# Kernel tuning notes

Hardware: AMD Instinct MI355X
Metric: run time of the kernel (lower is better)

The kernel has to match this reference:

```python
import jax, jax.numpy as jnp
import numpy as np

N = 50000      # nodes
E = 1600000    # edges (avg degree 32)
C_IN = 128
C_H = 128
C_OUT = 10
G = 512        # number of graphs in the batch


def setup_inputs() -> dict:
    key = jax.random.key(0)
    ks = jax.random.split(key, 16)
    x = jax.random.normal(ks[0], (N, C_IN), dtype=jnp.float32)
    edge_index = jax.random.randint(ks[1], (2, E), 0, N, dtype=jnp.int64)
    batch = jnp.sort(jax.random.randint(ks[2], (N,), 0, G, dtype=jnp.int64))

    def lin(k, fan_in, fan_out):
        lim = 1.0 / np.sqrt(fan_in)
        return jax.random.uniform(k, (fan_in, fan_out), jnp.float32, -lim, lim)

    return {
        "x": x, "edge_index": edge_index, "batch": batch,
        # conv1: c_in -> c_hidden
        "Wr1": lin(ks[3], C_IN, C_H), "br1": jnp.zeros((C_H,), jnp.float32),
        "Wo1": lin(ks[4], C_IN, C_H),
        # conv2: c_hidden -> 2*c_hidden
        "Wr2": lin(ks[5], C_H, 2 * C_H), "br2": jnp.zeros((2 * C_H,), jnp.float32),
        "Wo2": lin(ks[6], C_H, 2 * C_H),
        # conv3: 2*c_hidden -> c_hidden
        "Wr3": lin(ks[7], 2 * C_H, C_H), "br3": jnp.zeros((C_H,), jnp.float32),
        "Wo3": lin(ks[8], 2 * C_H, C_H),
        # head
        "W1": lin(ks[9], C_H, 4 * C_OUT), "b1": jnp.zeros((4 * C_OUT,), jnp.float32),
        "W2": lin(ks[10], 4 * C_OUT, C_OUT), "b2": jnp.zeros((C_OUT,), jnp.float32),
    }


def _graph_conv(x, src, dst, Wr, br, Wo):
    # PyG GraphConv: lin_rel(sum_{j in N(i)} x_j) + lin_root(x_i)
    agg = jax.ops.segment_sum(x[src], dst, num_segments=N)  # [N, F_in]
    return agg @ Wr + br + x @ Wo


def reference(x, edge_index, batch, Wr1, br1, Wo1, Wr2, br2, Wo2,
              Wr3, br3, Wo3, W1, b1, W2, b2):
    src, dst = edge_index[0], edge_index[1]
    h = jax.nn.relu(_graph_conv(x, src, dst, Wr1, br1, Wo1))
    h = jax.nn.relu(_graph_conv(h, src, dst, Wr2, br2, Wo2))
    h = _graph_conv(h, src, dst, Wr3, br3, Wo3)
    # global mean pool over graphs
    sums = jax.ops.segment_sum(h, batch, num_segments=G)            # [G, C_H]
    cnts = jax.ops.segment_sum(jnp.ones((N,), h.dtype), batch, num_segments=G)
    pooled = sums / jnp.maximum(cnts, 1.0)[:, None]
    # dropout is identity in eval mode
    out = pooled @ W1 + b1
    out = out @ W2 + b2
    return out
```

## Files before the change

kernel.cpp:

```cpp
#include <hip/hip_runtime.h>
#include <hip/hip_bf16.h>
#include <cstddef>

#define NN 50000
#define EE 1600000
#define GG 512
#define NB 196
#define BSTRIDE 16384
#define BCAP 10240
#define XBLKS 6250
#define SCBLKS 782

typedef unsigned int u32;
typedef unsigned short u16;
typedef __attribute__((ext_vector_type(8))) short frag_ab;
typedef __attribute__((ext_vector_type(4))) float frag_cd;

__device__ __forceinline__ void gl_lds16(const void* g, void* l) {
    __builtin_amdgcn_global_load_lds(
        (const __attribute__((address_space(1))) u32*)g,
        (__attribute__((address_space(3))) u32*)l, 16, 0, 0);
}
__device__ __forceinline__ float b2f_lo(u32 v) { return __uint_as_float(v << 16); }
__device__ __forceinline__ float b2f_hi(u32 v) { return __uint_as_float(v & 0xffff0000u); }
__device__ __forceinline__ float b2f(u32 v, int odd) { return odd ? b2f_hi(v) : b2f_lo(v); }
__device__ __forceinline__ u16 f2b(float x) {
    __hip_bfloat16 h = __float2bfloat16(x);
    return *(u16*)&h;
}
__device__ __forceinline__ u32 pack2(float lo, float hi) {
    return ((u32)f2b(hi) << 16) | f2b(lo);
}
__device__ __forceinline__ void acc2(float2& a, u32 v) {
    a.x += b2f_lo(v);
    a.y += b2f_hi(v);
}


__global__ __launch_bounds__(256) void bscatter_prep_kernel(
    const int* __restrict__ ei, int* __restrict__ bcnt, u32* __restrict__ pairs,
    const float* __restrict__ x, u16* __restrict__ ax,
    const float* __restrict__ Wr1, const float* __restrict__ Wo1,
    const float* __restrict__ Wr2, const float* __restrict__ Wo2,
    const float* __restrict__ Wr3, const float* __restrict__ Wo3,
    const float* __restrict__ br3,
    u16* __restrict__ BT1, u16* __restrict__ BT2, u16* __restrict__ BT3,
    float* __restrict__ bias3) {
    __shared__ int lcnt[NB];
    __shared__ int lbase[NB];
    __shared__ unsigned short lpos[2048];
    int bid = blockIdx.x, t = threadIdx.x;
    if (bid < SCBLKS) {
        int e0 = bid * 2048;
        u32 pk[8];
        int bk[8];
        for (int i = t; i < NB; i += 256) lcnt[i] = 0;
        __syncthreads();
#pragma unroll
        for (int i = 0; i < 8; ++i) {
            int e = e0 + i * 256 + t;
            if (e < EE) {
                int dst = ei[EE + e], src = ei[e];
                int b = dst >> 8;
                bk[i] = b;
                pk[i] = ((u32)src << 8) | (u32)(dst & 255);
                lpos[i * 256 + t] = (unsigned short)atomicAdd(&lcnt[b], 1);
            } else bk[i] = -1;
        }
        __syncthreads();
        for (int i = t; i < NB; i += 256) lbase[i] = atomicAdd(&bcnt[i], lcnt[i]);
        __syncthreads();
#pragma unroll
        for (int i = 0; i < 8; ++i) {
            if (bk[i] >= 0) {
                int pos = lbase[bk[i]] + (int)lpos[i * 256 + t];
                pairs[(size_t)bk[i] * BSTRIDE + pos] = pk[i];
            }
        }
    } else if (bid < SCBLKS + XBLKS) {
        int idx = (bid - SCBLKS) * 256 + t;
        int row = idx >> 5, q = idx & 31;
        float4 v = *(const float4*)(x + (size_t)row * 128 + q * 4);
        *(u32*)(ax + (size_t)row * 256 + 128 + q * 4) = pack2(v.x, v.y);
        *(u32*)(ax + (size_t)row * 256 + 128 + q * 4 + 2) = pack2(v.z, v.w);
    } else {
        int m = bid - SCBLKS - XBLKS;
        int k = t;
        BT2[m * 256 + k] = f2b(k < 128 ? Wr2[k * 256 + m] : Wo2[(k - 128) * 256 + m]);
        BT3[m * 256 + k] = f2b(m < 128 ? Wr3[k * 128 + m] : Wo3[k * 128 + (m - 128)]);
        if (m < 128)
            BT1[m * 256 + k] = f2b(k < 128 ? Wr1[k * 128 + m] : Wo1[(k - 128) * 128 + m]);
        if (k == 0) bias3[m] = (m < 128) ? 0.f : br3[m - 128];
    }
}


__global__ __launch_bounds__(512) void bfill_kernel(const u32* __restrict__ pairs,
                                                    const int* __restrict__ bcnt,
                                                    int* __restrict__ ofs,
                                                    int* __restrict__ srcl) {
    __shared__ int sc[256];
    __shared__ int cnts[256];
    __shared__ int lcnt[256];
    __shared__ int lcur[256];
    __shared__ int lbuf[BCAP];
    int b = blockIdx.x, t = threadIdx.x;
    if (t < 256) {
        int c = (t < NB) ? bcnt[t] : 0;
        cnts[t] = c;
        sc[t] = c;
        lcnt[t] = 0;
    }
    __syncthreads();
    for (int off = 1; off < 256; off <<= 1) {
        int v = (t >= off && t < 256) ? sc[t - off] : 0;
        __syncthreads();
        if (t < 256) sc[t] += v;
        __syncthreads();
    }
    int base = sc[b] - cnts[b];
    int span = cnts[b];
    const u32* pp = pairs + (size_t)b * BSTRIDE;
    for (int j = t; j < span; j += 512) atomicAdd(&lcnt[pp[j] & 255u], 1);
    __syncthreads();
    int nc = 0;
    if (t < 256) {
        nc = lcnt[t];
        sc[t] = nc;
    }
    __syncthreads();
    for (int off = 1; off < 256; off <<= 1) {
        int v = (t >= off && t < 256) ? sc[t - off] : 0;
        __syncthreads();
        if (t < 256) sc[t] += v;
        __syncthreads();
    }
    if (t < 256) {
        int excl = sc[t] - nc;
        int node = b * 256 + t;
        if (node < NN) ofs[node] = base + excl;
        lcur[t] = excl;
    }
    if (b == 0 && t == 256) ofs[NN] = EE;
    __syncthreads();
    for (int j = t; j < span; j += 512) {
        u32 p = pp[j];
        int pos = atomicAdd(&lcur[p & 255u], 1);
        int src = (int)(p >> 8);
        if (pos < BCAP) lbuf[pos] = src;
        else srcl[base + pos] = src;
    }
    __syncthreads();
    int lim = span < BCAP ? span : BCAP;
    for (int j = t; j < lim; j += 512) srcl[base + j] = lbuf[j];
}


__global__ __launch_bounds__(256) void pull_bf_kernel(const u32* __restrict__ Xu,
                                                      const int* __restrict__ ofs,
                                                      const int* __restrict__ srcl,
                                                      u32* __restrict__ outu) {
    int node = (blockIdx.x * 256 + threadIdx.x) >> 6;
    int lane = threadIdx.x & 63;
    int q = lane >> 4, l = lane & 15;
    int lo = ofs[node], hi = ofs[node + 1];
    float2 a0 = {0.f, 0.f}, a1 = {0.f, 0.f}, a2 = {0.f, 0.f}, a3 = {0.f, 0.f};
    int j = lo;
    for (; j + 15 < hi; j += 16) {
        int s0 = srcl[j + q], s1 = srcl[j + 4 + q];
        int s2 = srcl[j + 8 + q], s3 = srcl[j + 12 + q];
        uint4 v0 = *(const uint4*)(Xu + (size_t)s0 * 128 + l * 4);
        uint4 v1 = *(const uint4*)(Xu + (size_t)s1 * 128 + l * 4);
        uint4 v2 = *(const uint4*)(Xu + (size_t)s2 * 128 + l * 4);
        uint4 v3 = *(const uint4*)(Xu + (size_t)s3 * 128 + l * 4);
        acc2(a0, v0.x); acc2(a1, v0.y); acc2(a2, v0.z); acc2(a3, v0.w);
        acc2(a0, v1.x); acc2(a1, v1.y); acc2(a2, v1.z); acc2(a3, v1.w);
        acc2(a0, v2.x); acc2(a1, v2.y); acc2(a2, v2.z); acc2(a3, v2.w);
        acc2(a0, v3.x); acc2(a1, v3.y); acc2(a2, v3.z); acc2(a3, v3.w);
    }
    for (; j + 3 < hi; j += 4) {
        int s = srcl[j + q];
        uint4 v = *(const uint4*)(Xu + (size_t)s * 128 + l * 4);
        acc2(a0, v.x); acc2(a1, v.y); acc2(a2, v.z); acc2(a3, v.w);
    }
    if (j + q < hi) {
        int s = srcl[j + q];
        uint4 v = *(const uint4*)(Xu + (size_t)s * 128 + l * 4);
        acc2(a0, v.x); acc2(a1, v.y); acc2(a2, v.z); acc2(a3, v.w);
    }
    float acc[8] = {a0.x, a0.y, a1.x, a1.y, a2.x, a2.y, a3.x, a3.y};
#pragma unroll
    for (int i = 0; i < 8; ++i) {
        acc[i] += __shfl_xor(acc[i], 16, 64);
        acc[i] += __shfl_xor(acc[i], 32, 64);
    }
    if (q == 0) {
        uint4 r;
        r.x = pack2(acc[0], acc[1]);
        r.y = pack2(acc[2], acc[3]);
        r.z = pack2(acc[4], acc[5]);
        r.w = pack2(acc[6], acc[7]);
        *(uint4*)(outu + (size_t)node * 128 + l * 4) = r;
    }
}

__global__ __launch_bounds__(256) void pull3_kernel(const u32* __restrict__ Tu,
                                                    const int* __restrict__ ofs,
                                                    const int* __restrict__ srcl,
                                                    u32* __restrict__ h3u) {
    int node = (blockIdx.x * 256 + threadIdx.x) >> 6;
    int lane = threadIdx.x & 63;
    int q = lane >> 4, l = lane & 15;
    int lo = ofs[node], hi = ofs[node + 1];
    float2 a0 = {0.f, 0.f}, a1 = {0.f, 0.f}, a2 = {0.f, 0.f}, a3 = {0.f, 0.f};
    int j = lo;
    for (; j + 15 < hi; j += 16) {
        int s0 = srcl[j + q], s1 = srcl[j + 4 + q];
        int s2 = srcl[j + 8 + q], s3 = srcl[j + 12 + q];
        uint4 v0 = *(const uint4*)(Tu + (size_t)s0 * 128 + l * 4);
        uint4 v1 = *(const uint4*)(Tu + (size_t)s1 * 128 + l * 4);
        uint4 v2 = *(const uint4*)(Tu + (size_t)s2 * 128 + l * 4);
        uint4 v3 = *(const uint4*)(Tu + (size_t)s3 * 128 + l * 4);
        acc2(a0, v0.x); acc2(a1, v0.y); acc2(a2, v0.z); acc2(a3, v0.w);
        acc2(a0, v1.x); acc2(a1, v1.y); acc2(a2, v1.z); acc2(a3, v1.w);
        acc2(a0, v2.x); acc2(a1, v2.y); acc2(a2, v2.z); acc2(a3, v2.w);
        acc2(a0, v3.x); acc2(a1, v3.y); acc2(a2, v3.z); acc2(a3, v3.w);
    }
    for (; j + 3 < hi; j += 4) {
        int s = srcl[j + q];
        uint4 v = *(const uint4*)(Tu + (size_t)s * 128 + l * 4);
        acc2(a0, v.x); acc2(a1, v.y); acc2(a2, v.z); acc2(a3, v.w);
    }
    if (j + q < hi) {
        int s = srcl[j + q];
        uint4 v = *(const uint4*)(Tu + (size_t)s * 128 + l * 4);
        acc2(a0, v.x); acc2(a1, v.y); acc2(a2, v.z); acc2(a3, v.w);
    }
    float acc[8] = {a0.x, a0.y, a1.x, a1.y, a2.x, a2.y, a3.x, a3.y};
#pragma unroll
    for (int i = 0; i < 8; ++i) {
        acc[i] += __shfl_xor(acc[i], 16, 64);
        acc[i] += __shfl_xor(acc[i], 32, 64);
    }
    if (q == 0) {
        uint4 o = *(const uint4*)(Tu + (size_t)node * 128 + 64 + l * 4);
        acc[0] += b2f_lo(o.x); acc[1] += b2f_hi(o.x);
        acc[2] += b2f_lo(o.y); acc[3] += b2f_hi(o.y);
        acc[4] += b2f_lo(o.z); acc[5] += b2f_hi(o.z);
        acc[6] += b2f_lo(o.w); acc[7] += b2f_hi(o.w);
        uint4 r;
        r.x = pack2(acc[0], acc[1]);
        r.y = pack2(acc[2], acc[3]);
        r.z = pack2(acc[4], acc[5]);
        r.w = pack2(acc[6], acc[7]);
        *(uint4*)(h3u + (size_t)node * 64 + l * 4) = r;
    }
}


__global__ __launch_bounds__(256, 2) void gemm_bf_kernel(
    const u16* __restrict__ A, const u16* __restrict__ BT,
    const float* __restrict__ bias, u16* __restrict__ C,
    int ldc, int coloff, int relu) {
    __shared__ alignas(16) u16 As[128 * 32];
    __shared__ alignas(16) u16 Bs[128 * 32];
    const int t = threadIdx.x;
    const int lane = t & 63, wid = t >> 6;
    const int quad = lane >> 4, l16 = lane & 15;
    const int wm = wid >> 1, wn = wid & 1;
    const int row0 = blockIdx.y * 128, c0 = blockIdx.x * 128;

    frag_cd acc[4][4];
#pragma unroll
    for (int i = 0; i < 4; ++i)
#pragma unroll
        for (int j = 0; j < 4; ++j) acc[i][j] = (frag_cd)0.f;

    const int ca = t, cb = t + 256;
    const int ra = ca >> 2, oa = (ca & 3) * 8;
    const int rb = cb >> 2, ob = (cb & 3) * 8;
    const int garow = min(row0 + ra, NN - 1);
    const int gbrow = min(row0 + rb, NN - 1);
    const size_t gA1 = (size_t)garow * 256 + oa;
    const size_t gA2 = (size_t)gbrow * 256 + ob;
    const size_t gB1 = (size_t)(c0 + ra) * 256 + oa;
    const size_t gB2 = (size_t)(c0 + rb) * 256 + ob;

    for (int kk = 0; kk < 256; kk += 32) {
        __syncthreads();
        gl_lds16(A + gA1 + kk, &As[ca * 8]);
        gl_lds16(A + gA2 + kk, &As[cb * 8]);
        gl_lds16(BT + gB1 + kk, &Bs[ca * 8]);
        gl_lds16(BT + gB2 + kk, &Bs[cb * 8]);
        __syncthreads();

        frag_ab a[4], b[4];
#pragma unroll
        for (int mt = 0; mt < 4; ++mt)
            a[mt] = *(const frag_ab*)&As[(wm * 64 + mt * 16 + l16) * 32 + quad * 8];
#pragma unroll
        for (int nt = 0; nt < 4; ++nt)
            b[nt] = *(const frag_ab*)&Bs[(wn * 64 + nt * 16 + l16) * 32 + quad * 8];
#pragma unroll
        for (int mt = 0; mt < 4; ++mt)
#pragma unroll
            for (int nt = 0; nt < 4; ++nt)
                acc[mt][nt] = __builtin_amdgcn_mfma_f32_16x16x32_bf16(
                    a[mt], b[nt], acc[mt][nt], 0, 0, 0);
    }

#pragma unroll
    for (int nt = 0; nt < 4; ++nt) {
        int col = c0 + wn * 64 + nt * 16 + l16;
        float bv = bias[col];
#pragma unroll
        for (int mt = 0; mt < 4; ++mt) {
#pragma unroll
            for (int r = 0; r < 4; ++r) {
                int row = row0 + wm * 64 + mt * 16 + quad * 4 + r;
                if (row < NN) {
                    float v = acc[mt][nt][r] + bv;
                    if (relu) v = fmaxf(v, 0.f);
                    C[(size_t)row * ldc + coloff + col] = f2b(v);
                }
            }
        }
    }
}


__device__ inline int lower_bound_i(const int* a, int n, int v) {
    int lo = 0, hi = n;
    while (lo < hi) {
        int m = (lo + hi) >> 1;
        if (a[m] < v) lo = m + 1; else hi = m;
    }
    return lo;
}

__global__ __launch_bounds__(256) void pool_head_kernel(const u32* __restrict__ h3u,
                                                        const int* __restrict__ batch,
                                                        const float* __restrict__ W1,
                                                        const float* __restrict__ b1,
                                                        const float* __restrict__ W2,
                                                        const float* __restrict__ b2,
                                                        float* __restrict__ out) {
    __shared__ float ps[256];
    __shared__ float p[128];
    __shared__ float hid[40];
    int g = blockIdx.x, t = threadIdx.x;
    int c = t & 127, half = t >> 7;
    int w = c >> 1, odd = c & 1;
    int lo = lower_bound_i(batch, NN, g);
    int hi = lower_bound_i(batch, NN, g + 1);
    float s = 0.f;
    int i = lo + half;
    for (; i + 6 < hi; i += 8) {
        u32 v0 = h3u[(size_t)i * 64 + w];
        u32 v1 = h3u[(size_t)(i + 2) * 64 + w];
        u32 v2 = h3u[(size_t)(i + 4) * 64 + w];
        u32 v3 = h3u[(size_t)(i + 6) * 64 + w];
        s += (b2f(v0, odd) + b2f(v1, odd)) + (b2f(v2, odd) + b2f(v3, odd));
    }
    for (; i < hi; i += 2) s += b2f(h3u[(size_t)i * 64 + w], odd);
    ps[t] = s;
    __syncthreads();
    if (half == 0) p[c] = (ps[c] + ps[c + 128]) / fmaxf((float)(hi - lo), 1.f);
    __syncthreads();
    if (t < 40) {
        float v = b1[t];
        for (int k = 0; k < 128; ++k) v += p[k] * W1[k * 40 + t];
        hid[t] = v;
    }
    __syncthreads();
    if (t < 10) {
        float v = b2[t];
        for (int j = 0; j < 40; ++j) v += hid[j] * W2[j * 10 + t];
        out[g * 10 + t] = v;
    }
}


extern "C" void kernel_launch(void* const* d_in, const int* in_sizes, int n_in,
                              void* d_out, int out_size, void* d_ws, size_t ws_size,
                              hipStream_t stream) {
    const float* x   = (const float*)d_in[0];
    const int* ei    = (const int*)d_in[1];
    const int* batch = (const int*)d_in[2];
    const float* Wr1 = (const float*)d_in[3];
    const float* br1 = (const float*)d_in[4];
    const float* Wo1 = (const float*)d_in[5];
    const float* Wr2 = (const float*)d_in[6];
    const float* br2 = (const float*)d_in[7];
    const float* Wo2 = (const float*)d_in[8];
    const float* Wr3 = (const float*)d_in[9];
    const float* br3 = (const float*)d_in[10];
    const float* Wo3 = (const float*)d_in[11];
    const float* W1  = (const float*)d_in[12];
    const float* b1  = (const float*)d_in[13];
    const float* W2  = (const float*)d_in[14];
    const float* b2  = (const float*)d_in[15];
    float* out = (float*)d_out;

    char* ws = (char*)d_ws;
    size_t off = 0;
    auto alloc = [&](size_t bytes) {
        void* p = ws + off;
        off += (bytes + 255) & ~(size_t)255;
        return p;
    };
    int* ofs      = (int*)alloc((NN + 1) * sizeof(int));
    int* bcnt     = (int*)alloc(256 * sizeof(int));
    int* srcl     = (int*)alloc((size_t)EE * sizeof(int));
    u16* ax       = (u16*)alloc((size_t)NN * 256 * 2);
    u16* ah1      = (u16*)alloc((size_t)NN * 256 * 2);
    u16* h2       = (u16*)alloc((size_t)NN * 256 * 2);
    u16* t3o3     = (u16*)alloc((size_t)NN * 256 * 2);
    u16* h3       = (u16*)alloc((size_t)NN * 128 * 2);
    u16* BT1      = (u16*)alloc(128 * 256 * 2);
    u16* BT2      = (u16*)alloc(256 * 256 * 2);
    u16* BT3      = (u16*)alloc(256 * 256 * 2);
    float* bias3  = (float*)alloc(256 * sizeof(float));
    u32* pairs = (u32*)h2;

    hipMemsetAsync(bcnt, 0, 256 * sizeof(int), stream);

    bscatter_prep_kernel<<<SCBLKS + XBLKS + 256, 256, 0, stream>>>(
        ei, bcnt, pairs, x, ax, Wr1, Wo1, Wr2, Wo2, Wr3, Wo3, br3,
        BT1, BT2, BT3, bias3);
    bfill_kernel<<<NB, 512, 0, stream>>>(pairs, bcnt, ofs, srcl);

    pull_bf_kernel<<<NN * 64 / 256, 256, 0, stream>>>((const u32*)ax + 64, ofs, srcl, (u32*)ax);
    gemm_bf_kernel<<<dim3(1, 391), 256, 0, stream>>>(ax, BT1, br1, ah1, 256, 128, 1);
    pull_bf_kernel<<<NN * 64 / 256, 256, 0, stream>>>((const u32*)ah1 + 64, ofs, srcl, (u32*)ah1);
    gemm_bf_kernel<<<dim3(2, 391), 256, 0, stream>>>(ah1, BT2, br2, h2, 256, 0, 1);
    gemm_bf_kernel<<<dim3(2, 391), 256, 0, stream>>>(h2, BT3, bias3, t3o3, 256, 0, 0);
    pull3_kernel<<<NN * 64 / 256, 256, 0, stream>>>((const u32*)t3o3, ofs, srcl, (u32*)h3);

    pool_head_kernel<<<GG, 256, 0, stream>>>((const u32*)h3, batch, W1, b1, W2, b2, out);
}
```

Before: 364.3 us.

## Gather features in four column-sliced buffers and shrink edge source indices to 16-bit

Gathered node features now live in four column-slice buffers of 64 bytes per node, written by the prep and GEMM epilogues. Each pull block handles one slice for four nodes, which shrinks the random-access working set per pass so it fits in cache better. Source indices in the CSR list are stored as u16 to halve index traffic, but this silently truncates node ids at or above 65536; N=50000 fits. In exchange the GEMM epilogues do extra scattered stores and there are four times as many pull blocks.

```diff
diff --git a/kernel.cpp b/kernel.cpp
--- a/kernel.cpp
+++ b/kernel.cpp
@@ -39,7 +39,7 @@
 
 __global__ __launch_bounds__(256) void bscatter_prep_kernel(
     const int* __restrict__ ei, int* __restrict__ bcnt, u32* __restrict__ pairs,
-    const float* __restrict__ x, u16* __restrict__ ax,
+    const float* __restrict__ x, u16* __restrict__ ax, u32* __restrict__ G1,
     const float* __restrict__ Wr1, const float* __restrict__ Wo1,
     const float* __restrict__ Wr2, const float* __restrict__ Wo2,
     const float* __restrict__ Wr3, const float* __restrict__ Wo3,
@@ -81,8 +81,11 @@
         int idx = (bid - SCBLKS) * 256 + t;
         int row = idx >> 5, q = idx & 31;
         float4 v = *(const float4*)(x + (size_t)row * 128 + q * 4);
-        *(u32*)(ax + (size_t)row * 256 + 128 + q * 4) = pack2(v.x, v.y);
-        *(u32*)(ax + (size_t)row * 256 + 128 + q * 4 + 2) = pack2(v.z, v.w);
+        u32 w0 = pack2(v.x, v.y), w1 = pack2(v.z, v.w);
+        *(u32*)(ax + (size_t)row * 256 + 128 + q * 4) = w0;
+        *(u32*)(ax + (size_t)row * 256 + 128 + q * 4 + 2) = w1;
+        uint2 r; r.x = w0; r.y = w1;
+        *(uint2*)(G1 + ((size_t)(q >> 3) * NN + row) * 16 + ((2 * q) & 15)) = r;
     } else {
         int m = bid - SCBLKS - XBLKS;
         int k = t;
@@ -98,7 +101,7 @@
 __global__ __launch_bounds__(512) void bfill_kernel(const u32* __restrict__ pairs,
                                                     const int* __restrict__ bcnt,
                                                     int* __restrict__ ofs,
-                                                    int* __restrict__ srcl) {
+                                                    u16* __restrict__ srcl) {
     __shared__ int sc[256];
     __shared__ int cnts[256];
     __shared__ int lcnt[256];
@@ -148,120 +151,106 @@
         int pos = atomicAdd(&lcur[p & 255u], 1);
         int src = (int)(p >> 8);
         if (pos < BCAP) lbuf[pos] = src;
-        else srcl[base + pos] = src;
+        else srcl[base + pos] = (u16)src;
     }
     __syncthreads();
     int lim = span < BCAP ? span : BCAP;
-    for (int j = t; j < lim; j += 512) srcl[base + j] = lbuf[j];
-}
-
-
-__global__ __launch_bounds__(256) void pull_bf_kernel(const u32* __restrict__ Xu,
-                                                      const int* __restrict__ ofs,
-                                                      const int* __restrict__ srcl,
-                                                      u32* __restrict__ outu) {
-    int node = (blockIdx.x * 256 + threadIdx.x) >> 6;
+    for (int j = t; j < lim; j += 512) srcl[base + j] = (u16)lbuf[j];
+}
+
+
+__global__ __launch_bounds__(256) void pull_slice_kernel(const u32* __restrict__ G,
+                                                         const int* __restrict__ ofs,
+                                                         const u16* __restrict__ srcl,
+                                                         u32* __restrict__ outu,
+                                                         int rowstride) {
+    int s = blockIdx.x & 3;
+    int node = (blockIdx.x >> 2) * 4 + (threadIdx.x >> 6);
     int lane = threadIdx.x & 63;
-    int q = lane >> 4, l = lane & 15;
+    int q = lane >> 3, l = lane & 7;
+    const u32* Gs = G + (size_t)s * NN * 16;
     int lo = ofs[node], hi = ofs[node + 1];
-    float2 a0 = {0.f, 0.f}, a1 = {0.f, 0.f}, a2 = {0.f, 0.f}, a3 = {0.f, 0.f};
+    float2 a0 = {0.f, 0.f}, a1 = {0.f, 0.f};
     int j = lo;
     for (; j + 15 < hi; j += 16) {
-        int s0 = srcl[j + q], s1 = srcl[j + 4 + q];
-        int s2 = srcl[j + 8 + q], s3 = srcl[j + 12 + q];
-        uint4 v0 = *(const uint4*)(Xu + (size_t)s0 * 128 + l * 4);
-        uint4 v1 = *(const uint4*)(Xu + (size_t)s1 * 128 + l * 4);
-        uint4 v2 = *(const uint4*)(Xu + (size_t)s2 * 128 + l * 4);
-        uint4 v3 = *(const uint4*)(Xu + (size_t)s3 * 128 + l * 4);
-        acc2(a0, v0.x); acc2(a1, v0.y); acc2(a2, v0.z); acc2(a3, v0.w);
-        acc2(a0, v1.x); acc2(a1, v1.y); acc2(a2, v1.z); acc2(a3, v1.w);
-        acc2(a0, v2.x); acc2(a1, v2.y); acc2(a2, v2.z); acc2(a3, v2.w);
-        acc2(a0, v3.x); acc2(a1, v3.y); acc2(a2, v3.z); acc2(a3, v3.w);
-    }
-    for (; j + 3 < hi; j += 4) {
-        int s = srcl[j + q];
-        uint4 v = *(const uint4*)(Xu + (size_t)s * 128 + l * 4);
-        acc2(a0, v.x); acc2(a1, v.y); acc2(a2, v.z); acc2(a3, v.w);
-    }
-    if (j + q < hi) {
-        int s = srcl[j + q];
-        uint4 v = *(const uint4*)(Xu + (size_t)s * 128 + l * 4);
-        acc2(a0, v.x); acc2(a1, v.y); acc2(a2, v.z); acc2(a3, v.w);
-    }
-    float acc[8] = {a0.x, a0.y, a1.x, a1.y, a2.x, a2.y, a3.x, a3.y};
-#pragma unroll
-    for (int i = 0; i < 8; ++i) {
+        int s0 = srcl[j + q], s1 = srcl[j + 8 + q];
+        uint2 v0 = *(const uint2*)(Gs + (size_t)s0 * 16 + l * 2);
+        uint2 v1 = *(const uint2*)(Gs + (size_t)s1 * 16 + l * 2);
+        acc2(a0, v0.x); acc2(a1, v0.y);
+        acc2(a0, v1.x); acc2(a1, v1.y);
+    }
+    for (; j < hi; j += 8) {
+        if (j + q < hi) {
+            int s0 = srcl[j + q];
+            uint2 v = *(const uint2*)(Gs + (size_t)s0 * 16 + l * 2);
+            acc2(a0, v.x); acc2(a1, v.y);
+        }
+    }
+    float acc[4] = {a0.x, a0.y, a1.x, a1.y};
+#pragma unroll
+    for (int i = 0; i < 4; ++i) {
+        acc[i] += __shfl_xor(acc[i], 8, 64);
         acc[i] += __shfl_xor(acc[i], 16, 64);
         acc[i] += __shfl_xor(acc[i], 32, 64);
     }
     if (q == 0) {
-        uint4 r;
+        uint2 r;
         r.x = pack2(acc[0], acc[1]);
         r.y = pack2(acc[2], acc[3]);
-        r.z = pack2(acc[4], acc[5]);
-        r.w = pack2(acc[6], acc[7]);
-        *(uint4*)(outu + (size_t)node * 128 + l * 4) = r;
-    }
-}
-
-__global__ __launch_bounds__(256) void pull3_kernel(const u32* __restrict__ Tu,
-                                                    const int* __restrict__ ofs,
-                                                    const int* __restrict__ srcl,
-                                                    u32* __restrict__ h3u) {
-    int node = (blockIdx.x * 256 + threadIdx.x) >> 6;
+        *(uint2*)(outu + (size_t)node * rowstride + s * 16 + l * 2) = r;
+    }
+}
+
+__global__ __launch_bounds__(256) void pull3_slice_kernel(const u32* __restrict__ G,
+                                                          const int* __restrict__ ofs,
+                                                          const u16* __restrict__ srcl,
+                                                          const u32* __restrict__ o3u,
+                                                          u32* __restrict__ h3u) {
+    int s = blockIdx.x & 3;
+    int node = (blockIdx.x >> 2) * 4 + (threadIdx.x >> 6);
     int lane = threadIdx.x & 63;
-    int q = lane >> 4, l = lane & 15;
+    int q = lane >> 3, l = lane & 7;
+    const u32* Gs = G + (size_t)s * NN * 16;
     int lo = ofs[node], hi = ofs[node + 1];
-    float2 a0 = {0.f, 0.f}, a1 = {0.f, 0.f}, a2 = {0.f, 0.f}, a3 = {0.f, 0.f};
+    float2 a0 = {0.f, 0.f}, a1 = {0.f, 0.f};
     int j = lo;
     for (; j + 15 < hi; j += 16) {
-        int s0 = srcl[j + q], s1 = srcl[j + 4 + q];
-        int s2 = srcl[j + 8 + q], s3 = srcl[j + 12 + q];
-        uint4 v0 = *(const uint4*)(Tu + (size_t)s0 * 128 + l * 4);
-        uint4 v1 = *(const uint4*)(Tu + (size_t)s1 * 128 + l * 4);
-        uint4 v2 = *(const uint4*)(Tu + (size_t)s2 * 128 + l * 4);
-        uint4 v3 = *(const uint4*)(Tu + (size_t)s3 * 128 + l * 4);
-        acc2(a0, v0.x); acc2(a1, v0.y); acc2(a2, v0.z); acc2(a3, v0.w);
-        acc2(a0, v1.x); acc2(a1, v1.y); acc2(a2, v1.z); acc2(a3, v1.w);
-        acc2(a0, v2.x); acc2(a1, v2.y); acc2(a2, v2.z); acc2(a3, v2.w);
-        acc2(a0, v3.x); acc2(a1, v3.y); acc2(a2, v3.z); acc2(a3, v3.w);
-    }
-    for (; j + 3 < hi; j += 4) {
-        int s = srcl[j + q];
-        uint4 v = *(const uint4*)(Tu + (size_t)s * 128 + l * 4);
-        acc2(a0, v.x); acc2(a1, v.y); acc2(a2, v.z); acc2(a3, v.w);
-    }
-    if (j + q < hi) {
-        int s = srcl[j + q];
-        uint4 v = *(const uint4*)(Tu + (size_t)s * 128 + l * 4);
-        acc2(a0, v.x); acc2(a1, v.y); acc2(a2, v.z); acc2(a3, v.w);
-    }
-    float acc[8] = {a0.x, a0.y, a1.x, a1.y, a2.x, a2.y, a3.x, a3.y};
-#pragma unroll
-    for (int i = 0; i < 8; ++i) {
+        int s0 = srcl[j + q], s1 = srcl[j + 8 + q];
+        uint2 v0 = *(const uint2*)(Gs + (size_t)s0 * 16 + l * 2);
+        uint2 v1 = *(const uint2*)(Gs + (size_t)s1 * 16 + l * 2);
+        acc2(a0, v0.x); acc2(a1, v0.y);
+        acc2(a0, v1.x); acc2(a1, v1.y);
+    }
+    for (; j < hi; j += 8) {
+        if (j + q < hi) {
+            int s0 = srcl[j + q];
+            uint2 v = *(const uint2*)(Gs + (size_t)s0 * 16 + l * 2);
+            acc2(a0, v.x); acc2(a1, v.y);
+        }
+    }
+    float acc[4] = {a0.x, a0.y, a1.x, a1.y};
+#pragma unroll
+    for (int i = 0; i < 4; ++i) {
+        acc[i] += __shfl_xor(acc[i], 8, 64);
         acc[i] += __shfl_xor(acc[i], 16, 64);
         acc[i] += __shfl_xor(acc[i], 32, 64);
     }
     if (q == 0) {
-        uint4 o = *(const uint4*)(Tu + (size_t)node * 128 + 64 + l * 4);
+        uint2 o = *(const uint2*)(o3u + (size_t)node * 64 + s * 16 + l * 2);
         acc[0] += b2f_lo(o.x); acc[1] += b2f_hi(o.x);
         acc[2] += b2f_lo(o.y); acc[3] += b2f_hi(o.y);
-        acc[4] += b2f_lo(o.z); acc[5] += b2f_hi(o.z);
-        acc[6] += b2f_lo(o.w); acc[7] += b2f_hi(o.w);
-        uint4 r;
+        uint2 r;
         r.x = pack2(acc[0], acc[1]);
         r.y = pack2(acc[2], acc[3]);
-        r.z = pack2(acc[4], acc[5]);
-        r.w = pack2(acc[6], acc[7]);
-        *(uint4*)(h3u + (size_t)node * 64 + l * 4) = r;
+        *(uint2*)(h3u + (size_t)node * 64 + s * 16 + l * 2) = r;
     }
 }
 
 
 __global__ __launch_bounds__(256, 2) void gemm_bf_kernel(
     const u16* __restrict__ A, const u16* __restrict__ BT,
-    const float* __restrict__ bias, u16* __restrict__ C,
-    int ldc, int coloff, int relu) {
+    const float* __restrict__ bias, u16* __restrict__ Crow,
+    int ldc, int coloff, int rowlo, u16* __restrict__ Cslc, int slchi, int relu) {
     __shared__ alignas(16) u16 As[128 * 32];
     __shared__ alignas(16) u16 Bs[128 * 32];
     const int t = threadIdx.x;
@@ -313,6 +302,7 @@
     for (int nt = 0; nt < 4; ++nt) {
         int col = c0 + wn * 64 + nt * 16 + l16;
         float bv = bias[col];
+        int w = col >> 1, s = w >> 4, wis = w & 15, odd = col & 1;
 #pragma unroll
         for (int mt = 0; mt < 4; ++mt) {
 #pragma unroll
@@ -321,7 +311,11 @@
                 if (row < NN) {
                     float v = acc[mt][nt][r] + bv;
                     if (relu) v = fmaxf(v, 0.f);
-                    C[(size_t)row * ldc + coloff + col] = f2b(v);
+                    u16 bb = f2b(v);
+                    if (col >= rowlo)
+                        Crow[(size_t)row * ldc + coloff + col] = bb;
+                    if (col < slchi)
+                        Cslc[(((size_t)s * NN + row) * 16 + wis) * 2 + odd] = bb;
                 }
             }
         }
@@ -411,11 +405,14 @@
     };
     int* ofs      = (int*)alloc((NN + 1) * sizeof(int));
     int* bcnt     = (int*)alloc(256 * sizeof(int));
-    int* srcl     = (int*)alloc((size_t)EE * sizeof(int));
+    u16* srcl     = (u16*)alloc((size_t)EE * 2);
     u16* ax       = (u16*)alloc((size_t)NN * 256 * 2);
     u16* ah1      = (u16*)alloc((size_t)NN * 256 * 2);
     u16* h2       = (u16*)alloc((size_t)NN * 256 * 2);
-    u16* t3o3     = (u16*)alloc((size_t)NN * 256 * 2);
+    u32* G1       = (u32*)alloc((size_t)4 * NN * 16 * 4);
+    u32* G2       = (u32*)alloc((size_t)4 * NN * 16 * 4);
+    u32* G3       = (u32*)alloc((size_t)4 * NN * 16 * 4);
+    u16* o3       = (u16*)alloc((size_t)NN * 128 * 2);
     u16* h3       = (u16*)alloc((size_t)NN * 128 * 2);
     u16* BT1      = (u16*)alloc(128 * 256 * 2);
     u16* BT2      = (u16*)alloc(256 * 256 * 2);
@@ -426,16 +423,19 @@
     hipMemsetAsync(bcnt, 0, 256 * sizeof(int), stream);
 
     bscatter_prep_kernel<<<SCBLKS + XBLKS + 256, 256, 0, stream>>>(
-        ei, bcnt, pairs, x, ax, Wr1, Wo1, Wr2, Wo2, Wr3, Wo3, br3,
+        ei, bcnt, pairs, x, ax, G1, Wr1, Wo1, Wr2, Wo2, Wr3, Wo3, br3,
         BT1, BT2, BT3, bias3);
     bfill_kernel<<<NB, 512, 0, stream>>>(pairs, bcnt, ofs, srcl);
 
-    pull_bf_kernel<<<NN * 64 / 256, 256, 0, stream>>>((const u32*)ax + 64, ofs, srcl, (u32*)ax);
-    gemm_bf_kernel<<<dim3(1, 391), 256, 0, stream>>>(ax, BT1, br1, ah1, 256, 128, 1);
-    pull_bf_kernel<<<NN * 64 / 256, 256, 0, stream>>>((const u32*)ah1 + 64, ofs, srcl, (u32*)ah1);
-    gemm_bf_kernel<<<dim3(2, 391), 256, 0, stream>>>(ah1, BT2, br2, h2, 256, 0, 1);
-    gemm_bf_kernel<<<dim3(2, 391), 256, 0, stream>>>(h2, BT3, bias3, t3o3, 256, 0, 0);
-    pull3_kernel<<<NN * 64 / 256, 256, 0, stream>>>((const u32*)t3o3, ofs, srcl, (u32*)h3);
+    pull_slice_kernel<<<NN, 256, 0, stream>>>(G1, ofs, srcl, (u32*)ax, 128);
+    gemm_bf_kernel<<<dim3(1, 391), 256, 0, stream>>>(ax, BT1, br1,
+                                                     ah1, 256, 128, 0, (u16*)G2, 128, 1);
+    pull_slice_kernel<<<NN, 256, 0, stream>>>(G2, ofs, srcl, (u32*)ah1, 128);
+    gemm_bf_kernel<<<dim3(2, 391), 256, 0, stream>>>(ah1, BT2, br2,
+                                                     h2, 256, 0, 0, nullptr, 0, 1);
+    gemm_bf_kernel<<<dim3(2, 391), 256, 0, stream>>>(h2, BT3, bias3,
+                                                     o3, 128, -128, 128, (u16*)G3, 128, 0);
+    pull3_slice_kernel<<<NN, 256, 0, stream>>>(G3, ofs, srcl, (const u32*)o3, (u32*)h3);
 
     pool_head_kernel<<<GG, 256, 0, stream>>>((const u32*)h3, batch, W1, b1, W2, b2, out);
 }
```

Result: slower. 470.6 us (+29.2%).
